# Optimization experiments

Hardware: AMD Instinct MI355X
Metric: run time of the kernel (lower is better)

## Reference

```python
import jax, jax.numpy as jnp
import numpy as np

N_NODES = 50000
N_EDGES = 200000
MUL0 = 64   # multiplicity of 0e irreps in in1
MUL1 = 32   # multiplicity of 1o irreps in in1
IN1_SIZE = MUL0 + 3 * MUL1            # 160
IN2_SIZE = 1 + 3                      # sph harmonics l=0,1
W_SIZE = MUL0 + MUL0 + MUL1 + MUL1 + MUL1  # 224, one weight per u per path
OUT_SIZE = (MUL0 + MUL1) + 3 * (MUL0 + MUL1 + MUL1)  # 480
INV_SQRT3 = 0.5773502691896258  # CG norm for 1x1->0 (dot)
INV_SQRT2 = 0.7071067811865476  # CG norm for 1x1->1 (cross)


def setup_inputs() -> dict:
    key = jax.random.key(0)
    k1, k2, k3, k4, k5 = jax.random.split(key, 5)
    return {
        'in1': jax.random.normal(k1, (N_NODES, IN1_SIZE), dtype=jnp.float32),
        'in2': jax.random.normal(k2, (N_EDGES, IN2_SIZE), dtype=jnp.float32),
        'weight': jax.random.normal(k3, (N_EDGES, W_SIZE), dtype=jnp.float32) * 0.1,
        'per_edge_src': jax.random.randint(k4, (N_EDGES,), 0, N_NODES, dtype=jnp.int64),
        'per_edge_dst': jax.random.randint(k5, (N_EDGES,), 0, N_NODES, dtype=jnp.int64),
    }


def _tp_messages(in1, in2, weight, per_edge_src):
    # Gather source node features per edge: [E, IN1_SIZE]
    x = in1[per_edge_src]
    s1 = x[:, :MUL0]                          # [E, MUL0]   scalars (0e)
    v1 = x[:, MUL0:].reshape(-1, MUL1, 3)     # [E, MUL1,3] vectors (1o)
    y0 = in2[:, :1]                            # [E, 1]
    y1 = in2[:, 1:4]                           # [E, 3]
    # per-edge uvu weights, one per u channel per path
    o = 0
    w1 = weight[:, o:o + MUL0]; o += MUL0
    w2 = weight[:, o:o + MUL0]; o += MUL0
    w3 = weight[:, o:o + MUL1]; o += MUL1
    w4 = weight[:, o:o + MUL1]; o += MUL1
    w5 = weight[:, o:o + MUL1]; o += MUL1
    # path 1: 0e x 0e -> 0e
    p1 = w1 * s1 * y0                                             # [E, MUL0]
    # path 4: 1o x 1o -> 0e (dot)
    p4 = w4 * jnp.einsum('eui,ei->eu', v1, y1) * INV_SQRT3        # [E, MUL1]
    # path 2: 0e x 1o -> 1o
    p2 = (w2 * s1)[:, :, None] * y1[:, None, :]                   # [E, MUL0,3]
    # path 3: 1o x 0e -> 1o
    p3 = w3[:, :, None] * v1 * y0[:, None, :]                     # [E, MUL1,3]
    # path 5: 1o x 1o -> 1o (cross)
    p5 = w5[:, :, None] * jnp.cross(v1, y1[:, None, :]) * INV_SQRT2  # [E, MUL1,3]
    return jnp.concatenate([
        p1, p4,
        p2.reshape(-1, 3 * MUL0),
        p3.reshape(-1, 3 * MUL1),
        p5.reshape(-1, 3 * MUL1),
    ], axis=1)  # [E, OUT_SIZE]


def reference(in1, in2, weight, per_edge_src, per_edge_dst):
    msg = _tp_messages(in1, in2, weight, per_edge_src)
    # scatter-add messages to destination nodes (out starts at zeros in the kernel)
    return jax.ops.segment_sum(msg, per_edge_dst, num_segments=in1.shape[0])
```

## Files before the change

### kernel.cpp

```cpp
#include <hip/hip_runtime.h>

#define N_NODES 50000
#define N_EDGES 200000
#define IN1_SIZE 160
#define W_SIZE 224
#define OUT_SIZE 480
#define INV_SQRT3 0.5773502691896258f
#define INV_SQRT2 0.7071067811865476f

__global__ void hist_kernel(const int* __restrict__ dst, int* __restrict__ counts) {
    int i = blockIdx.x * blockDim.x + threadIdx.x;
    if (i < N_EDGES) atomicAdd(&counts[dst[i]], 1);
}

__global__ __launch_bounds__(1024) void scan_blocks_kernel(
    const int* __restrict__ counts, int* __restrict__ offsets,
    int* __restrict__ partials)
{
    __shared__ int sm[1024];
    const int t = threadIdx.x;
    const int gid = blockIdx.x * 1024 + t;
    const int v = (gid < N_NODES) ? counts[gid] : 0;
    sm[t] = v;
    __syncthreads();
    for (int off = 1; off < 1024; off <<= 1) {
        int a = (t >= off) ? sm[t - off] : 0;
        __syncthreads();
        sm[t] += a;
        __syncthreads();
    }
    if (gid < N_NODES) offsets[gid] = sm[t] - v;
    if (t == 1023) partials[blockIdx.x] = sm[1023];
}

__global__ __launch_bounds__(1024) void add_partials_kernel(
    const int* __restrict__ partials, int* __restrict__ offsets,
    int* __restrict__ cursor)
{
    const int blk = blockIdx.x;
    const int gid = blk * 1024 + threadIdx.x;
    int s = 0;
    for (int j = 0; j < blk; ++j) s += partials[j];
    if (gid < N_NODES) {
        const int o = offsets[gid] + s;
        offsets[gid] = o;
        cursor[gid]  = o;
    }
}

__global__ void fill_kernel(const int* __restrict__ dst, const int* __restrict__ src,
                            const float4* __restrict__ in2,
                            int* __restrict__ cursor, int* __restrict__ edgelist,
                            int* __restrict__ ss, float4* __restrict__ ys) {
    int i = blockIdx.x * blockDim.x + threadIdx.x;
    if (i < N_EDGES) {
        int pos = atomicAdd(&cursor[dst[i]], 1);
        edgelist[pos] = i;
        ss[pos] = src[i];
        ys[pos] = in2[i];
    }
}

__global__ __launch_bounds__(256) void tp_node4b_kernel(
    const float*  __restrict__ in1,
    const float*  __restrict__ weight,
    const int*    __restrict__ offsets,
    const int*    __restrict__ edgelist,
    const int*    __restrict__ ss,
    const float4* __restrict__ ys,
    float*        __restrict__ out)
{
    __shared__ float sm[4][512];
    const int wave = threadIdx.x >> 6;
    const int lane = threadIdx.x & 63;
    const int n = blockIdx.x;
    const int u = lane & 31;
    const int h = lane >> 5;

    const int start = offsets[n];
    const int end   = (n + 1 < N_NODES) ? offsets[n + 1] : N_EDGES;

    float acc0 = 0.f, acc1 = 0.f, acc2 = 0.f, acc3 = 0.f;
    float acc4 = 0.f, acc5 = 0.f, acc6 = 0.f, acc7 = 0.f;

    for (int p = start + wave; p < end; p += 4) {
        const int pu = __builtin_amdgcn_readfirstlane(p);
        const int e0 = edgelist[pu];
        const int s0 = ss[pu];
        const float4 yv = ys[pu];
        const float y0 = yv.x, yx = yv.y, yy = yv.z, yz = yv.w;

        const float* __restrict__ x = in1 + (long)s0 * IN1_SIZE;
        const float* __restrict__ w = weight + (long)e0 * W_SIZE;

        const float xs = x[lane];
        const float a  = x[64 + lane];
        const float b  = x[128 + u];
        const float w1 = w[lane];
        const float w2 = w[64 + lane];
        const float c  = w[128 + lane];
        const float d  = w[192 + u];

        float v0, v1, v2;
        {
            const int j0 = 3 * u;
            const float a0 = __shfl(a, j0 & 63);
            const float b0 = __shfl(b, j0 & 63);
            v0 = (j0 < 64) ? a0 : b0;
            const int j1 = j0 + 1;
            const float a1 = __shfl(a, j1 & 63);
            const float b1 = __shfl(b, j1 & 63);
            v1 = (j1 < 64) ? a1 : b1;
            const int j2 = j0 + 2;
            const float a2 = __shfl(a, j2 & 63);
            const float b2 = __shfl(b, j2 & 63);
            v2 = (j2 < 64) ? a2 : b2;
        }
        const float w3 = __shfl(c, u);
        const float w4 = __shfl(c, u + 32);
        const float w5 = __shfl(d, u);

        acc0 += w1 * xs * y0;
        const float sw2 = w2 * xs;
        acc1 += sw2 * yx;
        acc2 += sw2 * yy;
        acc3 += sw2 * yz;
        if (h == 0) {
            acc4 += w4 * (v0 * yx + v1 * yy + v2 * yz) * INV_SQRT3;
            const float wy = w3 * y0;
            acc5 += wy * v0;
            acc6 += wy * v1;
            acc7 += wy * v2;
        } else {
            const float wc = w5 * INV_SQRT2;
            acc5 += wc * (v1 * yz - v2 * yy);
            acc6 += wc * (v2 * yx - v0 * yz);
            acc7 += wc * (v0 * yy - v1 * yx);
        }
    }

    float* smw = &sm[wave][0];
    smw[0 * 64 + lane] = acc0;
    smw[1 * 64 + lane] = acc1;
    smw[2 * 64 + lane] = acc2;
    smw[3 * 64 + lane] = acc3;
    smw[4 * 64 + lane] = acc4;
    smw[5 * 64 + lane] = acc5;
    smw[6 * 64 + lane] = acc6;
    smw[7 * 64 + lane] = acc7;
    __syncthreads();

    float* __restrict__ row = out + (long)n * OUT_SIZE;
    #pragma unroll
    for (int r = 0; r < 2; ++r) {
        const int s  = threadIdx.x + 256 * r;
        const int j  = s >> 6;
        const int l  = s & 63;
        const int uu = l & 31;
        const int hh = l >> 5;
        const float v = sm[0][s] + sm[1][s] + sm[2][s] + sm[3][s];
        int off;
        bool valid = true;
        if (j == 0)        off = l;
        else if (j <= 3)   off = 96 + 3 * l + (j - 1);
        else if (j == 4) { off = 64 + uu; valid = (hh == 0); }
        else               off = (hh ? 384 : 288) + 3 * uu + (j - 5);
        if (valid) row[off] = v;
    }
}

__global__ void zero_out_kernel(float4* __restrict__ out, int n4) {
    const float4 z = make_float4(0.f, 0.f, 0.f, 0.f);
    for (int i = blockIdx.x * blockDim.x + threadIdx.x; i < n4;
         i += gridDim.x * blockDim.x) out[i] = z;
}

__device__ __forceinline__ float edge_val(
    int idx, const float* __restrict__ x, const float* __restrict__ w,
    float y0, float y1x, float y1y, float y1z)
{
    if (idx < 64) {
        return w[idx] * x[idx] * y0;
    } else if (idx < 96) {
        const int u = idx - 64;
        const float a0 = x[64 + 3 * u], a1 = x[65 + 3 * u], a2 = x[66 + 3 * u];
        return w[160 + u] * (a0 * y1x + a1 * y1y + a2 * y1z) * INV_SQRT3;
    } else if (idx < 288) {
        const int t = idx - 96;
        const int i = t / 3;
        const int k = t - 3 * i;
        const float yk = (k == 0) ? y1x : (k == 1) ? y1y : y1z;
        return w[64 + i] * x[i] * yk;
    } else if (idx < 384) {
        const int t = idx - 288;
        const int u = t / 3;
        const int k = t - 3 * u;
        return w[128 + u] * x[64 + 3 * u + k] * y0;
    } else {
        const int t = idx - 384;
        const int u = t / 3;
        const int k = t - 3 * u;
        const float a0 = x[64 + 3 * u], a1 = x[65 + 3 * u], a2 = x[66 + 3 * u];
        float cc;
        if (k == 0)      cc = a1 * y1z - a2 * y1y;
        else if (k == 1) cc = a2 * y1x - a0 * y1z;
        else             cc = a0 * y1y - a1 * y1x;
        return w[192 + u] * cc * INV_SQRT2;
    }
}

__global__ __launch_bounds__(256) void tp_scatter_kernel(
    const float* __restrict__ in1, const float* __restrict__ in2,
    const float* __restrict__ weight,
    const int* __restrict__ src, const int* __restrict__ dst,
    float* __restrict__ out)
{
    const int wave = threadIdx.x >> 6;
    const int lane = threadIdx.x & 63;
    const int e = blockIdx.x * 4 + wave;
    if (e >= N_EDGES) return;
    const int sn = src[e];
    const int dn = dst[e];
    const float* __restrict__ x = in1 + (long)sn * IN1_SIZE;
    const float* __restrict__ w = weight + (long)e * W_SIZE;
    const float y0  = in2[e * 4 + 0];
    const float y1x = in2[e * 4 + 1];
    const float y1y = in2[e * 4 + 2];
    const float y1z = in2[e * 4 + 3];
    float* __restrict__ o = out + (long)dn * OUT_SIZE;
    #pragma unroll
    for (int j = 0; j < 8; ++j) {
        const int idx = lane + (j << 6);
        if (idx < OUT_SIZE)
            atomicAdd(o + idx, edge_val(idx, x, w, y0, y1x, y1y, y1z));
    }
}

extern "C" void kernel_launch(void* const* d_in, const int* in_sizes, int n_in,
                              void* d_out, int out_size, void* d_ws, size_t ws_size,
                              hipStream_t stream) {
    const float* in1    = (const float*)d_in[0];
    const float* in2    = (const float*)d_in[1];
    const float* weight = (const float*)d_in[2];
    const int*   src    = (const int*)d_in[3];
    const int*   dst    = (const int*)d_in[4];
    float* out = (float*)d_out;

    const size_t need = (size_t)N_EDGES * 16 +
                        (size_t)(3 * N_NODES + 2 * N_EDGES + 64) * sizeof(int);
    if (ws_size >= need) {
        float4* ys     = (float4*)d_ws;
        int* counts    = (int*)(ys + N_EDGES);
        int* offsets   = counts + N_NODES;
        int* cursor    = offsets + N_NODES;
        int* edgelist  = cursor + N_NODES;
        int* ss        = edgelist + N_EDGES;
        int* partials  = ss + N_EDGES;

        const int nblk = (N_NODES + 1023) / 1024;

        hipMemsetAsync(counts, 0, N_NODES * sizeof(int), stream);
        hist_kernel<<<(N_EDGES + 255) / 256, 256, 0, stream>>>(dst, counts);
        scan_blocks_kernel<<<nblk, 1024, 0, stream>>>(counts, offsets, partials);
        add_partials_kernel<<<nblk, 1024, 0, stream>>>(partials, offsets, cursor);
        fill_kernel<<<(N_EDGES + 255) / 256, 256, 0, stream>>>(
            dst, src, (const float4*)in2, cursor, edgelist, ss, ys);

        tp_node4b_kernel<<<N_NODES, 256, 0, stream>>>(
            in1, weight, offsets, edgelist, ss, ys, out);
    } else {
        const int n4 = out_size / 4;
        zero_out_kernel<<<2048, 256, 0, stream>>>((float4*)out, n4);
        tp_scatter_kernel<<<(N_EDGES + 3) / 4, 256, 0, stream>>>(
            in1, in2, weight, src, dst, out);
    }
}
```

Before: 122.8 us.

## Process fixed 8-edge chunks per wave with segmented flush and boundary atomics

Replaces the one-block-per-node reduction with fixed chunks of 8 dst-sorted edges per wave. Each wave accumulates runs of edges that share a destination and flushes them with plain stores, using atomics only when a run crosses a chunk boundary. A zero_rows kernel clears only the rows that are empty or split across chunks, and the edge metadata (edge id, src, dst) is packed into one int4. The aim is to remove the load imbalance and idle waves that come from variable node degree, and the shared-memory reduction. The cost is an extra kernel, some atomics at boundaries, and the correctness of the clearing and write-vs-atomic logic depends on the chunk alignment.

Measured after the change: 219.6 us. 78.9% more time.

```diff
diff --git a/kernel.cpp b/kernel.cpp
--- a/kernel.cpp
+++ b/kernel.cpp
@@ -5,6 +5,7 @@
 #define IN1_SIZE 160
 #define W_SIZE 224
 #define OUT_SIZE 480
+#define RCHUNK 8
 #define INV_SQRT3 0.5773502691896258f
 #define INV_SQRT2 0.7071067811865476f
 
@@ -50,78 +51,139 @@
 
 __global__ void fill_kernel(const int* __restrict__ dst, const int* __restrict__ src,
                             const float4* __restrict__ in2,
-                            int* __restrict__ cursor, int* __restrict__ edgelist,
-                            int* __restrict__ ss, float4* __restrict__ ys) {
+                            int* __restrict__ cursor, int4* __restrict__ meta,
+                            float4* __restrict__ ys) {
     int i = blockIdx.x * blockDim.x + threadIdx.x;
     if (i < N_EDGES) {
-        int pos = atomicAdd(&cursor[dst[i]], 1);
-        edgelist[pos] = i;
-        ss[pos] = src[i];
+        int d = dst[i];
+        int pos = atomicAdd(&cursor[d], 1);
+        meta[pos] = make_int4(i, src[i], d, 0);
         ys[pos] = in2[i];
     }
 }
 
-__global__ __launch_bounds__(256) void tp_node4b_kernel(
+__global__ __launch_bounds__(256) void zero_rows_kernel(
+    const int* __restrict__ counts, const int* __restrict__ offsets,
+    float* __restrict__ out)
+{
+    const int wave = threadIdx.x >> 6;
+    const int lane = threadIdx.x & 63;
+    const int n = blockIdx.x * 4 + wave;
+    if (n >= N_NODES) return;
+    const int cnt = counts[n];
+    const int start = offsets[n];
+    const bool nz = (cnt == 0) || ((start >> 3) != ((start + cnt - 1) >> 3));
+    if (!nz) return;
+    float* __restrict__ row = out + (long)n * OUT_SIZE;
+    #pragma unroll
+    for (int j = 0; j < 8; ++j) {
+        const int idx = lane + (j << 6);
+        if (idx < OUT_SIZE) row[idx] = 0.f;
+    }
+}
+
+__global__ __launch_bounds__(256) void tp_chunk8_kernel(
     const float*  __restrict__ in1,
     const float*  __restrict__ weight,
-    const int*    __restrict__ offsets,
-    const int*    __restrict__ edgelist,
-    const int*    __restrict__ ss,
+    const int4*   __restrict__ meta,
     const float4* __restrict__ ys,
     float*        __restrict__ out)
 {
-    __shared__ float sm[4][512];
-    const int wave = threadIdx.x >> 6;
     const int lane = threadIdx.x & 63;
-    const int n = blockIdx.x;
     const int u = lane & 31;
     const int h = lane >> 5;
-
-    const int start = offsets[n];
-    const int end   = (n + 1 < N_NODES) ? offsets[n + 1] : N_EDGES;
+    const int wid = blockIdx.x * 4 + (threadIdx.x >> 6);
+    const int p0 = __builtin_amdgcn_readfirstlane(wid * RCHUNK);
+    if (p0 >= N_EDGES) return;
+
+    int4   m_[RCHUNK];
+    float4 y_[RCHUNK];
+    #pragma unroll
+    for (int t = 0; t < RCHUNK; ++t) {
+        m_[t] = meta[p0 + t];
+        y_[t] = ys[p0 + t];
+    }
+    const int d_prev = (p0 > 0) ? meta[p0 - 1].z : -1;
+    const int d_next = (p0 + RCHUNK < N_EDGES) ? meta[p0 + RCHUNK].z : -1;
+    const bool head_shared = (d_prev == m_[0].z);
+    const bool tail_shared = (d_next == m_[RCHUNK - 1].z);
+
+    float xs_[RCHUNK], a_[RCHUNK], bd_[RCHUNK], w1_[RCHUNK], w2_[RCHUNK], c_[RCHUNK];
+    #pragma unroll
+    for (int t = 0; t < RCHUNK; ++t) {
+        const float* __restrict__ x = in1 + (long)m_[t].y * IN1_SIZE;
+        const float* __restrict__ w = weight + (long)m_[t].x * W_SIZE;
+        xs_[t] = x[lane];
+        a_[t]  = x[64 + lane];
+        bd_[t] = (h == 0) ? x[128 + u] : w[192 + u];
+        w1_[t] = w[lane];
+        w2_[t] = w[64 + lane];
+        c_[t]  = w[128 + lane];
+    }
+
+    const int off0 = lane;
+    const int off1 = 96 + 3 * lane;
+    const int off4 = 64 + u;
+    const int off5 = (h ? 384 : 288) + 3 * u;
 
     float acc0 = 0.f, acc1 = 0.f, acc2 = 0.f, acc3 = 0.f;
     float acc4 = 0.f, acc5 = 0.f, acc6 = 0.f, acc7 = 0.f;
 
-    for (int p = start + wave; p < end; p += 4) {
-        const int pu = __builtin_amdgcn_readfirstlane(p);
-        const int e0 = edgelist[pu];
-        const int s0 = ss[pu];
-        const float4 yv = ys[pu];
-        const float y0 = yv.x, yx = yv.y, yy = yv.z, yz = yv.w;
-
-        const float* __restrict__ x = in1 + (long)s0 * IN1_SIZE;
-        const float* __restrict__ w = weight + (long)e0 * W_SIZE;
-
-        const float xs = x[lane];
-        const float a  = x[64 + lane];
-        const float b  = x[128 + u];
-        const float w1 = w[lane];
-        const float w2 = w[64 + lane];
-        const float c  = w[128 + lane];
-        const float d  = w[192 + u];
-
+    auto flush = [&](int node, bool use_atomic) {
+        float* __restrict__ row = out + (long)node * OUT_SIZE;
+        if (use_atomic) {
+            atomicAdd(row + off0,     acc0);
+            atomicAdd(row + off1,     acc1);
+            atomicAdd(row + off1 + 1, acc2);
+            atomicAdd(row + off1 + 2, acc3);
+            if (h == 0) atomicAdd(row + off4, acc4);
+            atomicAdd(row + off5,     acc5);
+            atomicAdd(row + off5 + 1, acc6);
+            atomicAdd(row + off5 + 2, acc7);
+        } else {
+            row[off0]     = acc0;
+            row[off1]     = acc1;
+            row[off1 + 1] = acc2;
+            row[off1 + 2] = acc3;
+            if (h == 0) row[off4] = acc4;
+            row[off5]     = acc5;
+            row[off5 + 1] = acc6;
+            row[off5 + 2] = acc7;
+        }
+        acc0 = acc1 = acc2 = acc3 = acc4 = acc5 = acc6 = acc7 = 0.f;
+    };
+
+    int cur = m_[0].z;
+    bool first = true;
+
+    #pragma unroll
+    for (int t = 0; t < RCHUNK; ++t) {
+        if (m_[t].z != cur) {
+            flush(cur, first && head_shared);
+            first = false;
+            cur = m_[t].z;
+        }
+        const float y0 = y_[t].x, yx = y_[t].y, yy = y_[t].z, yz = y_[t].w;
+
+        const int j0 = 3 * u;
         float v0, v1, v2;
         {
-            const int j0 = 3 * u;
-            const float a0 = __shfl(a, j0 & 63);
-            const float b0 = __shfl(b, j0 & 63);
-            v0 = (j0 < 64) ? a0 : b0;
-            const int j1 = j0 + 1;
-            const float a1 = __shfl(a, j1 & 63);
-            const float b1 = __shfl(b, j1 & 63);
-            v1 = (j1 < 64) ? a1 : b1;
-            const int j2 = j0 + 2;
-            const float a2 = __shfl(a, j2 & 63);
-            const float b2 = __shfl(b, j2 & 63);
-            v2 = (j2 < 64) ? a2 : b2;
+            const float s0a = __shfl(a_[t], j0 & 63);
+            const float s0b = __shfl(bd_[t], j0 & 63);
+            v0 = (j0 < 64) ? s0a : s0b;
+            const float s1a = __shfl(a_[t], (j0 + 1) & 63);
+            const float s1b = __shfl(bd_[t], (j0 + 1) & 63);
+            v1 = (j0 + 1 < 64) ? s1a : s1b;
+            const float s2a = __shfl(a_[t], (j0 + 2) & 63);
+            const float s2b = __shfl(bd_[t], (j0 + 2) & 63);
+            v2 = (j0 + 2 < 64) ? s2a : s2b;
         }
-        const float w3 = __shfl(c, u);
-        const float w4 = __shfl(c, u + 32);
-        const float w5 = __shfl(d, u);
-
-        acc0 += w1 * xs * y0;
-        const float sw2 = w2 * xs;
+        const float w3 = __shfl(c_[t], u);
+        const float w4 = __shfl(c_[t], u + 32);
+        const float w5 = __shfl(bd_[t], 32 + u);
+
+        acc0 += w1_[t] * xs_[t] * y0;
+        const float sw2 = w2_[t] * xs_[t];
         acc1 += sw2 * yx;
         acc2 += sw2 * yy;
         acc3 += sw2 * yz;
@@ -138,35 +200,7 @@
             acc7 += wc * (v0 * yy - v1 * yx);
         }
     }
-
-    float* smw = &sm[wave][0];
-    smw[0 * 64 + lane] = acc0;
-    smw[1 * 64 + lane] = acc1;
-    smw[2 * 64 + lane] = acc2;
-    smw[3 * 64 + lane] = acc3;
-    smw[4 * 64 + lane] = acc4;
-    smw[5 * 64 + lane] = acc5;
-    smw[6 * 64 + lane] = acc6;
-    smw[7 * 64 + lane] = acc7;
-    __syncthreads();
-
-    float* __restrict__ row = out + (long)n * OUT_SIZE;
-    #pragma unroll
-    for (int r = 0; r < 2; ++r) {
-        const int s  = threadIdx.x + 256 * r;
-        const int j  = s >> 6;
-        const int l  = s & 63;
-        const int uu = l & 31;
-        const int hh = l >> 5;
-        const float v = sm[0][s] + sm[1][s] + sm[2][s] + sm[3][s];
-        int off;
-        bool valid = true;
-        if (j == 0)        off = l;
-        else if (j <= 3)   off = 96 + 3 * l + (j - 1);
-        else if (j == 4) { off = 64 + uu; valid = (hh == 0); }
-        else               off = (hh ? 384 : 288) + 3 * uu + (j - 5);
-        if (valid) row[off] = v;
-    }
+    flush(cur, (first && head_shared) || tail_shared);
 }
 
 __global__ void zero_out_kernel(float4* __restrict__ out, int n4) {
@@ -246,16 +280,15 @@
     const int*   dst    = (const int*)d_in[4];
     float* out = (float*)d_out;
 
-    const size_t need = (size_t)N_EDGES * 16 +
-                        (size_t)(3 * N_NODES + 2 * N_EDGES + 64) * sizeof(int);
+    const size_t need = (size_t)N_EDGES * 32 +
+                        (size_t)(3 * N_NODES + 64) * sizeof(int);
     if (ws_size >= need) {
         float4* ys     = (float4*)d_ws;
-        int* counts    = (int*)(ys + N_EDGES);
+        int4*   meta   = (int4*)(ys + N_EDGES);
+        int* counts    = (int*)(meta + N_EDGES);
         int* offsets   = counts + N_NODES;
         int* cursor    = offsets + N_NODES;
-        int* edgelist  = cursor + N_NODES;
-        int* ss        = edgelist + N_EDGES;
-        int* partials  = ss + N_EDGES;
+        int* partials  = cursor + N_NODES;
 
         const int nblk = (N_NODES + 1023) / 1024;
 
@@ -264,10 +297,12 @@
         scan_blocks_kernel<<<nblk, 1024, 0, stream>>>(counts, offsets, partials);
         add_partials_kernel<<<nblk, 1024, 0, stream>>>(partials, offsets, cursor);
         fill_kernel<<<(N_EDGES + 255) / 256, 256, 0, stream>>>(
-            dst, src, (const float4*)in2, cursor, edgelist, ss, ys);
-
-        tp_node4b_kernel<<<N_NODES, 256, 0, stream>>>(
-            in1, weight, offsets, edgelist, ss, ys, out);
+            dst, src, (const float4*)in2, cursor, meta, ys);
+        zero_rows_kernel<<<(N_NODES + 3) / 4, 256, 0, stream>>>(counts, offsets, out);
+
+        const int nwaves = N_EDGES / RCHUNK;
+        tp_chunk8_kernel<<<(nwaves + 3) / 4, 256, 0, stream>>>(
+            in1, weight, meta, ys, out);
     } else {
         const int n4 = out_size / 4;
         zero_out_kernel<<<2048, 256, 0, stream>>>((float4*)out, n4);
```
